# Kernel optimization log

Measured on AMD Instinct MI355X. Metric: run time of the kernel, lower is better.

Reference implementation:

```python
import jax, jax.numpy as jnp
import numpy as np

HEAD = 4
EPS = 1e-12


def _l2norm(x, axis):
    # torch F.normalize: x / max(||x||_2, eps)
    return x / jnp.maximum(jnp.linalg.norm(x, axis=axis, keepdims=True), EPS)


def setup_inputs() -> dict:
    key = jax.random.key(0)
    ks = jax.random.split(key, 12)
    n, t, c, h, w = 2, 7, 96, 96, 96
    inp = {
        "curr_feat": jax.random.normal(ks[0], (n, c, h, w), jnp.float32),
        "index_feat_set_s1": jax.random.normal(ks[1], (n, t, c, h, w), jnp.float32),
        "anchor_feat": jax.random.normal(ks[2], (n, c, h, w), jnp.float32),
        "sparse_feat_set_s1": jax.random.normal(ks[3], (n, t, c, h, w), jnp.float32),
        "sparse_feat_set_s2": jax.random.normal(ks[4], (n, t, c, h, w), jnp.float32),
        "sparse_feat_set_s3": jax.random.normal(ks[5], (n, t, c, h, w), jnp.float32),
        # absolute pixel coordinates (x,y interleaved per frame), mostly in-bounds
        # with a little overshoot to exercise zeros padding of grid_sample
        "location_feat": jax.random.uniform(ks[6], (n, t * 2, h, w), jnp.float32, minval=-2.0, maxval=float(w) + 1.0),
        "proj_w": 0.02 * jax.random.normal(ks[7], (c, c), jnp.float32),
        "proj_b": jnp.zeros((c,), jnp.float32),
        "fusion_w": 0.02 * jax.random.normal(ks[8], (c, 3 * c), jnp.float32),
        "fusion_b": jnp.zeros((c,), jnp.float32),
    }
    return inp


def reference(curr_feat, index_feat_set_s1, anchor_feat, sparse_feat_set_s1,
              sparse_feat_set_s2, sparse_feat_set_s3, location_feat,
              proj_w, proj_b, fusion_w, fusion_b):
    n, c, h, w = anchor_feat.shape
    t = sparse_feat_set_s1.shape[1]
    hd = c // HEAD
    hw = h * w

    # ---- flow-guided nearest grid_sample (align_corners=True, zeros pad) ----
    loc = location_feat.reshape(n, t, 2, h, w)  # (n,t,2,h,w): [x, y] pixel coords
    gx = 2.0 * loc[:, :, 0] / max(w - 1, 1) - 1.0
    gy = 2.0 * loc[:, :, 1] / max(h - 1, 1) - 1.0
    ix = jnp.round((gx + 1.0) * 0.5 * (w - 1))  # nearest (round-half-even, as torch)
    iy = jnp.round((gy + 1.0) * 0.5 * (h - 1))
    valid = (ix >= 0) & (ix <= w - 1) & (iy >= 0) & (iy <= h - 1)
    lin = (jnp.clip(iy, 0, h - 1).astype(jnp.int32) * w
           + jnp.clip(ix, 0, w - 1).astype(jnp.int32)).reshape(n, t, 1, hw)
    vmask = valid.reshape(n, t, 1, hw)

    def sample(f):  # f: (n,t,c,h,w) -> gathered (n,t,c,hw)
        g = jnp.take_along_axis(f.reshape(n, t, c, hw), lin, axis=3)
        return jnp.where(vmask, g, 0.0)

    samp1 = sample(sparse_feat_set_s1)
    samp2 = sample(sparse_feat_set_s2)
    samp3 = sample(sparse_feat_set_s3)
    sampi = sample(index_feat_set_s1)

    # ---- per-pixel multi-head max-correlation over t frames ----
    # queries: normalize over full channel dim c BEFORE splitting into heads
    q = _l2norm(curr_feat.reshape(n, c, hw).transpose(0, 2, 1), -1).reshape(n, hw, HEAD, hd)
    k = _l2norm(sampi.transpose(0, 3, 1, 2), -1).reshape(n, hw, t, HEAD, hd)
    scores = jnp.einsum('npthd,nphd->npht', k, q)  # scale == 1.0 in mode='max'
    corr_soft = jnp.max(scores, axis=3)     # (n,hw,head)
    corr_index = jnp.argmax(scores, axis=3)  # (n,hw,head), first-max like torch

    soft_img = jnp.broadcast_to(corr_soft[..., None], (n, hw, HEAD, hd)) \
                  .reshape(n, h, w, c).transpose(0, 3, 1, 2)  # (n,c,h,w)
    idx = jnp.broadcast_to(corr_index[..., None], (n, hw, HEAD, hd)) \
             .reshape(n, hw, c).transpose(0, 2, 1)[:, None]  # (n,1,c,hw)

    def pick(samp):  # select winning frame per (channel-group, pixel)
        return jnp.take_along_axis(samp, idx, axis=1)[:, 0].reshape(n, c, h, w)

    cat = jnp.concatenate([pick(samp1), pick(samp2), pick(samp3)], axis=1)  # (n,3c,h,w)
    out = jnp.einsum('ndhw,cd->nchw', cat, fusion_w) + fusion_b[None, :, None, None]
    out = out * soft_img
    out = jnp.einsum('nchw,dc->ndhw', out, proj_w) + proj_b[None, :, None, None]
    return out + anchor_feat
```

## Files before the change

### kernel.cpp

```cpp
#include <hip/hip_runtime.h>
#include <hip/hip_bf16.h>

#define N_    2
#define T_    7
#define C_    96
#define H_    96
#define W_    96
#define HW_   9216
#define HEAD_ 4
#define HD_   24
#define C3_   288
#define P_    16
#define QP_   100
#define CATP_ 292
#define NBLK_ (N_ * (HW_ / P_))
#define PLANES_ 14
#define CHUNK_  64
#define NCHUNK_ 144

typedef unsigned int u32;

__device__ __forceinline__ float bits2f(u32 b) {
    union { u32 u; float f; } x; x.u = b; return x.f;
}

__device__ __forceinline__ unsigned short f2bf(float f) {
    union { __hip_bfloat16 h; unsigned short s; } u;
    u.h = __float2bfloat16(f);
    return u.s;
}

template<bool BF16>
__device__ __forceinline__ float ld1(const void* p, int i) {
    if constexpr (BF16) return bits2f(((u32)((const unsigned short*)p)[i]) << 16);
    else                return ((const float*)p)[i];
}

template<bool BF16>
__device__ __forceinline__ void ld4w(const void* p, int i, float w[4]) {
    if constexpr (BF16) {
        const uint2 u = ((const uint2*)p)[i >> 2];
        w[0] = bits2f(u.x << 16);
        w[1] = bits2f(u.x & 0xFFFF0000u);
        w[2] = bits2f(u.y << 16);
        w[3] = bits2f(u.y & 0xFFFF0000u);
    } else {
        const float4 v = *((const float4*)((const float*)p + i));
        w[0] = v.x; w[1] = v.y; w[2] = v.z; w[3] = v.w;
    }
}

template<bool BF16>
__device__ __forceinline__ void st4w(void* p, int i, const float v[4]) {
    if constexpr (BF16) {
        uint2 w;
        w.x = (u32)f2bf(v[0]) | ((u32)f2bf(v[1]) << 16);
        w.y = (u32)f2bf(v[2]) | ((u32)f2bf(v[3]) << 16);
        ((uint2*)p)[i >> 2] = w;
    } else {
        *((float4*)((float*)p + i)) = make_float4(v[0], v[1], v[2], v[3]);
    }
}

__global__ void detect_dtype_kernel(const u32* __restrict__ w, int* __restrict__ flag) {
    u32 x = w[threadIdx.x];
    u32 f = x & 0x7FFFu;
    int inwin = (f >= 0x3A00u) && (f <= 0x4200u);
    unsigned long long m = __ballot(inwin);
    if (threadIdx.x == 0) flag[0] = (__popcll(m) >= 40) ? 1 : 0;
}

template<bool BF16>
__global__ __launch_bounds__(256) void transp_kernel(
    const void* __restrict__ a0, const void* __restrict__ a1,
    const void* __restrict__ a2, const void* __restrict__ a3,
    void* __restrict__ dstb, unsigned long long szb, const int* __restrict__ flag)
{
    if ((*flag != 0) != BF16) return;
    const int arr = blockIdx.y;
    const void* src = (arr == 0) ? a0 : (arr == 1) ? a1 : (arr == 2) ? a2 : a3;
    void* dst = (char*)dstb + (unsigned long long)arr * szb;
    const int bx = blockIdx.x;
    const int pl = bx / NCHUNK_;
    const int x0 = (bx - pl * NCHUNK_) * CHUNK_;
    const int tid = threadIdx.x;
    if constexpr (BF16) {
        __shared__ unsigned short tile[C_][CHUNK_ + 2];
        const unsigned short* s = (const unsigned short*)src;
        unsigned short* d = (unsigned short*)dst;
        for (int i = tid; i < C_ * (CHUNK_ / 4); i += 256) {
            int ch = i >> 4, xq = i & 15;
            const ushort4 v = *((const ushort4*)(s + (pl * C_ + ch) * HW_ + x0 + 4 * xq));
            tile[ch][4 * xq + 0] = v.x; tile[ch][4 * xq + 1] = v.y;
            tile[ch][4 * xq + 2] = v.z; tile[ch][4 * xq + 3] = v.w;
        }
        __syncthreads();
        for (int i = tid; i < CHUNK_ * (C_ / 4); i += 256) {
            int p = i / 24, cq = i - p * 24;
            ushort4 v;
            v.x = tile[4 * cq + 0][p]; v.y = tile[4 * cq + 1][p];
            v.z = tile[4 * cq + 2][p]; v.w = tile[4 * cq + 3][p];
            *((ushort4*)(d + (pl * HW_ + x0 + p) * C_ + 4 * cq)) = v;
        }
    } else {
        __shared__ float tile[C_][CHUNK_ + 1];
        const float* s = (const float*)src;
        float* d = (float*)dst;
        for (int i = tid; i < C_ * (CHUNK_ / 4); i += 256) {
            int ch = i >> 4, xq = i & 15;
            const float4 v = *((const float4*)(s + (pl * C_ + ch) * HW_ + x0 + 4 * xq));
            tile[ch][4 * xq + 0] = v.x; tile[ch][4 * xq + 1] = v.y;
            tile[ch][4 * xq + 2] = v.z; tile[ch][4 * xq + 3] = v.w;
        }
        __syncthreads();
        for (int i = tid; i < CHUNK_ * (C_ / 4); i += 256) {
            int p = i / 24, cq = i - p * 24;
            float4 v;
            v.x = tile[4 * cq + 0][p]; v.y = tile[4 * cq + 1][p];
            v.z = tile[4 * cq + 2][p]; v.w = tile[4 * cq + 3][p];
            *((float4*)(d + (pl * HW_ + x0 + p) * C_ + 4 * cq)) = v;
        }
    }
}

template<bool BF16, int MODE>
__global__ __launch_bounds__(256) void traj_main(
    const void* __restrict__ curr, const void* __restrict__ idxf,
    const void* __restrict__ anchor, const void* __restrict__ s1,
    const void* __restrict__ s2, const void* __restrict__ s3,
    const void* __restrict__ loc, const void* __restrict__ pw,
    const void* __restrict__ pb, const void* __restrict__ fw,
    const void* __restrict__ fb, void* __restrict__ outp,
    const int* __restrict__ flag,
    const void* __restrict__ kT, const void* __restrict__ s1T,
    const void* __restrict__ s2T, const void* __restrict__ s3T)
{
    if ((*flag != 0) != BF16) return;

    __shared__ __align__(16) float s_u[P_ * CATP_];
    __shared__ __align__(16) float s_mid[P_][QP_];
    __shared__ int   s_lin[T_][P_];
    __shared__ float s_red[P_][8];
    __shared__ float s_best[P_][HEAD_];
    __shared__ int   s_bidx[P_][HEAD_];
    __shared__ float s_inv[P_];

#define S_Q(pp, ch)  s_u[(pp) * QP_ + (ch)]
#define S_K(pp, ch)  s_u[P_ * QP_ + (pp) * QP_ + (ch)]
#define S_CAT(pp, d) s_u[(pp) * CATP_ + (d)]

    const int tid = threadIdx.x;
    const int b  = blockIdx.x;
    const int nn = b / (HW_ / P_);
    const int p0 = (b - nn * (HW_ / P_)) * P_;

    if (tid < T_ * P_) {
        int t = tid / P_, pp = tid - t * P_;
        int p = p0 + pp;
        float x = ld1<BF16>(loc, (nn * 2 * T_ + 2 * t    ) * HW_ + p);
        float y = ld1<BF16>(loc, (nn * 2 * T_ + 2 * t + 1) * HW_ + p);
        float gx = 2.0f * x / 95.0f - 1.0f;
        float gy = 2.0f * y / 95.0f - 1.0f;
        float fx = (gx + 1.0f) * 0.5f * 95.0f;
        float fy = (gy + 1.0f) * 0.5f * 95.0f;
        float ix = rintf(fx), iy = rintf(fy);
        bool v = (ix >= 0.0f) && (ix <= 95.0f) && (iy >= 0.0f) && (iy <= 95.0f);
        s_lin[t][pp] = v ? ((int)iy * W_ + (int)ix) : -1;
    }
    if (tid >= 128 && tid < 128 + P_ * HEAD_) {
        int q = tid - 128;
        s_best[q >> 2][q & 3] = -3.0e38f; s_bidx[q >> 2][q & 3] = 0;
    }

    for (int i = tid; i < C_ * (P_ / 4); i += 256) {
        int ch = i >> 2, pq = i & 3;
        float w[4];
        ld4w<BF16>(curr, (nn * C_ + ch) * HW_ + p0 + 4 * pq, w);
        S_Q(4 * pq + 0, ch) = w[0]; S_Q(4 * pq + 1, ch) = w[1];
        S_Q(4 * pq + 2, ch) = w[2]; S_Q(4 * pq + 3, ch) = w[3];
    }
    __syncthreads();

    if (tid < P_ * 8) {
        int pp = tid >> 3, j = tid & 7;
        float s = 0.f;
        #pragma unroll
        for (int k = 0; k < 12; ++k) { float v = S_Q(pp, j * 12 + k); s += v * v; }
        s_red[pp][j] = s;
    }
    __syncthreads();
    if (tid < P_) {
        float s = 0.f;
        #pragma unroll
        for (int j = 0; j < 8; ++j) s += s_red[tid][j];
        s_inv[tid] = 1.0f / fmaxf(sqrtf(s), 1e-12f);
    }
    __syncthreads();
    for (int i = tid; i < C_ * P_; i += 256) {
        int pp = i & (P_ - 1), ch = i >> 4;
        S_Q(pp, ch) *= s_inv[pp];
    }

    for (int t = 0; t < T_; ++t) {
        __syncthreads();
        if constexpr (MODE >= 1) {
            for (int i = tid; i < 24 * P_; i += 256) {
                int pp = i / 24, j = i - pp * 24;
                int lin = s_lin[t][pp];
                float w[4] = {0.f, 0.f, 0.f, 0.f};
                if (lin >= 0) ld4w<BF16>(kT, ((nn * T_ + t) * HW_ + lin) * C_ + 4 * j, w);
                *((float4*)&S_K(pp, 4 * j)) = make_float4(w[0], w[1], w[2], w[3]);
            }
        } else {
            for (int i = tid; i < C_ * P_; i += 256) {
                int ch = i / P_, pp = i - ch * P_;
                int lin = s_lin[t][pp];
                S_K(pp, ch) = (lin >= 0) ? ld1<BF16>(idxf, ((nn * T_ + t) * C_ + ch) * HW_ + lin) : 0.0f;
            }
        }
        __syncthreads();
        if (tid < P_ * 8) {
            int pp = tid >> 3, j = tid & 7;
            float s = 0.f;
            #pragma unroll
            for (int k = 0; k < 12; ++k) { float v = S_K(pp, j * 12 + k); s += v * v; }
            s_red[pp][j] = s;
        }
        __syncthreads();
        if (tid < P_) {
            float s = 0.f;
            #pragma unroll
            for (int j = 0; j < 8; ++j) s += s_red[tid][j];
            s_inv[tid] = 1.0f / fmaxf(sqrtf(s), 1e-12f);
        }
        __syncthreads();
        if (tid < P_ * HEAD_) {
            int pp = tid >> 2, h = tid & 3;
            float s = 0.f;
            #pragma unroll
            for (int dq = 0; dq < 6; ++dq) {
                const float4 kv = *((const float4*)&S_K(pp, h * HD_ + 4 * dq));
                const float4 qv = *((const float4*)&S_Q(pp, h * HD_ + 4 * dq));
                s += kv.x * qv.x; s += kv.y * qv.y; s += kv.z * qv.z; s += kv.w * qv.w;
            }
            s *= s_inv[pp];
            if (s > s_best[pp][h]) { s_best[pp][h] = s; s_bidx[pp][h] = t; }
        }
    }
    __syncthreads();

    if constexpr (MODE == 2) {
        for (int i = tid; i < 72 * P_; i += 256) {
            int pp = i / 72, j = i - pp * 72;
            int set = j / 24, jj = j - set * 24;
            int d0 = set * C_ + 4 * jj;
            int bt = s_bidx[pp][jj / 6];
            int lin = s_lin[bt][pp];
            float w[4] = {0.f, 0.f, 0.f, 0.f};
            if (lin >= 0) {
                const void* sp = (set == 0) ? s1T : (set == 1) ? s2T : s3T;
                ld4w<BF16>(sp, ((nn * T_ + bt) * HW_ + lin) * C_ + 4 * jj, w);
            }
            *((float4*)&S_CAT(pp, d0)) = make_float4(w[0], w[1], w[2], w[3]);
        }
    } else {
        for (int i = tid; i < C3_ * P_; i += 256) {
            int pp = i / C3_, d = i - pp * C3_;
            int set = d / C_, ch = d - set * C_;
            int h = ch / HD_;
            int bt = s_bidx[pp][h];
            int lin = s_lin[bt][pp];
            float v = 0.f;
            if (lin >= 0) {
                const void* sp = (set == 0) ? s1 : (set == 1) ? s2 : s3;
                v = ld1<BF16>(sp, ((nn * T_ + bt) * C_ + ch) * HW_ + lin);
            }
            S_CAT(pp, d) = v;
        }
    }
    __syncthreads();

    if (tid < 96) {
        const int cq = tid >> 2, pq = tid & 3;
        const int co0 = cq * 4, px0 = pq * 4;
        float acc[4][4];
        #pragma unroll
        for (int r = 0; r < 4; ++r)
            #pragma unroll
            for (int k = 0; k < 4; ++k) acc[r][k] = 0.f;
        for (int d = 0; d < C3_; d += 4) {
            float4 cv[4];
            #pragma unroll
            for (int k = 0; k < 4; ++k) cv[k] = *((const float4*)&S_CAT(px0 + k, d));
            #pragma unroll
            for (int r = 0; r < 4; ++r) {
                float w[4]; ld4w<BF16>(fw, (co0 + r) * C3_ + d, w);
                #pragma unroll
                for (int k = 0; k < 4; ++k)
                    acc[r][k] += w[0] * cv[k].x + w[1] * cv[k].y + w[2] * cv[k].z + w[3] * cv[k].w;
            }
        }
        const int hh = co0 / HD_;
        #pragma unroll
        for (int r = 0; r < 4; ++r) {
            float fbv = ld1<BF16>(fb, co0 + r);
            #pragma unroll
            for (int k = 0; k < 4; ++k)
                s_mid[px0 + k][co0 + r] = (acc[r][k] + fbv) * s_best[px0 + k][hh];
        }
    }
    __syncthreads();

    if (tid < 96) {
        const int dq = tid >> 2, pq = tid & 3;
        const int do0 = dq * 4, px0 = pq * 4;
        float acc[4][4];
        #pragma unroll
        for (int r = 0; r < 4; ++r)
            #pragma unroll
            for (int k = 0; k < 4; ++k) acc[r][k] = 0.f;
        for (int c = 0; c < C_; c += 4) {
            float4 mv[4];
            #pragma unroll
            for (int k = 0; k < 4; ++k) mv[k] = *((const float4*)&s_mid[px0 + k][c]);
            #pragma unroll
            for (int r = 0; r < 4; ++r) {
                float w[4]; ld4w<BF16>(pw, (do0 + r) * C_ + c, w);
                #pragma unroll
                for (int k = 0; k < 4; ++k)
                    acc[r][k] += w[0] * mv[k].x + w[1] * mv[k].y + w[2] * mv[k].z + w[3] * mv[k].w;
            }
        }
        #pragma unroll
        for (int r = 0; r < 4; ++r) {
            float pbv = ld1<BF16>(pb, do0 + r);
            float av[4];
            ld4w<BF16>(anchor, (nn * C_ + do0 + r) * HW_ + p0 + px0, av);
            float res[4];
            #pragma unroll
            for (int k = 0; k < 4; ++k) res[k] = acc[r][k] + pbv + av[k];
            st4w<BF16>(outp, (nn * C_ + do0 + r) * HW_ + p0 + px0, res);
        }
    }
#undef S_Q
#undef S_K
#undef S_CAT
}

extern "C" void kernel_launch(void* const* d_in, const int* in_sizes, int n_in,
                              void* d_out, int out_size, void* d_ws, size_t ws_size,
                              hipStream_t stream) {
    (void)in_sizes; (void)n_in; (void)out_size;
    int* flag = (int*)d_ws;
    char* wsb = (char*)d_ws;
    const unsigned long long SZB = (unsigned long long)N_ * T_ * HW_ * C_ * 4ull;
    void* kT  = wsb + 512;
    void* s1T = wsb + 512 + SZB;
    void* s2T = wsb + 512 + 2 * SZB;
    void* s3T = wsb + 512 + 3 * SZB;
    const int mode = (ws_size >= 512 + 4 * SZB) ? 2 : (ws_size >= 512 + SZB) ? 1 : 0;

    detect_dtype_kernel<<<1, 64, 0, stream>>>((const u32*)d_in[0], flag);

    if (mode >= 1) {
        dim3 tg(PLANES_ * NCHUNK_, (mode == 2) ? 4 : 1);
        transp_kernel<true ><<<tg, 256, 0, stream>>>(d_in[1], d_in[3], d_in[4], d_in[5], kT, SZB, flag);
        transp_kernel<false><<<tg, 256, 0, stream>>>(d_in[1], d_in[3], d_in[4], d_in[5], kT, SZB, flag);
    }

    dim3 grid(NBLK_), block(256);
#define LAUNCH_MODE(M) \
    traj_main<true,  M><<<grid, block, 0, stream>>>(d_in[0], d_in[1], d_in[2], d_in[3], d_in[4], \
        d_in[5], d_in[6], d_in[7], d_in[8], d_in[9], d_in[10], d_out, flag, kT, s1T, s2T, s3T);  \
    traj_main<false, M><<<grid, block, 0, stream>>>(d_in[0], d_in[1], d_in[2], d_in[3], d_in[4], \
        d_in[5], d_in[6], d_in[7], d_in[8], d_in[9], d_in[10], d_out, flag, kT, s1T, s2T, s3T)

    if (mode == 2)      { LAUNCH_MODE(2); }
    else if (mode == 1) { LAUNCH_MODE(1); }
    else                { LAUNCH_MODE(0); }
#undef LAUNCH_MODE
}
```

Measured before the change: 341.5 us.

## Drop sparse-set transposes and fold dtype detection into each kernel

Removes the transpose of the three sparse feature sets (mode 2), so the gather now reads 288 scalar values per pixel straight from the channel-major layout instead of vectorized channel-last loads. This saves the full read-plus-write pass over three large tensors, at the cost of scattered, uncoalesced gathers. It also drops the separate dtype-detection launch and the paired bf16/fp32 launches: each block now detects the dtype itself and branches, which cuts kernel launches but adds a 64-element read and a barrier per block.

```diff
diff --git a/kernel.cpp b/kernel.cpp
--- a/kernel.cpp
+++ b/kernel.cpp
@@ -62,30 +62,27 @@
     }
 }
 
-__global__ void detect_dtype_kernel(const u32* __restrict__ w, int* __restrict__ flag) {
-    u32 x = w[threadIdx.x];
-    u32 f = x & 0x7FFFu;
-    int inwin = (f >= 0x3A00u) && (f <= 0x4200u);
-    unsigned long long m = __ballot(inwin);
-    if (threadIdx.x == 0) flag[0] = (__popcll(m) >= 40) ? 1 : 0;
+__device__ __forceinline__ bool block_detect_bf16(const u32* __restrict__ w,
+                                                  int tid, int* s_flag) {
+    if (tid < 64) {
+        u32 x = w[tid];
+        u32 f = x & 0x7FFFu;
+        int inwin = (f >= 0x3A00u) && (f <= 0x4200u);
+        unsigned long long m = __ballot(inwin);
+        if (tid == 0) *s_flag = (__popcll(m) >= 40) ? 1 : 0;
+    }
+    __syncthreads();
+    return *s_flag != 0;
 }
 
 template<bool BF16>
-__global__ __launch_bounds__(256) void transp_kernel(
-    const void* __restrict__ a0, const void* __restrict__ a1,
-    const void* __restrict__ a2, const void* __restrict__ a3,
-    void* __restrict__ dstb, unsigned long long szb, const int* __restrict__ flag)
-{
-    if ((*flag != 0) != BF16) return;
-    const int arr = blockIdx.y;
-    const void* src = (arr == 0) ? a0 : (arr == 1) ? a1 : (arr == 2) ? a2 : a3;
-    void* dst = (char*)dstb + (unsigned long long)arr * szb;
-    const int bx = blockIdx.x;
+__device__ __forceinline__ void transp_body(const void* __restrict__ src,
+                                            void* __restrict__ dst,
+                                            int bx, int tid, char* tileraw) {
     const int pl = bx / NCHUNK_;
     const int x0 = (bx - pl * NCHUNK_) * CHUNK_;
-    const int tid = threadIdx.x;
     if constexpr (BF16) {
-        __shared__ unsigned short tile[C_][CHUNK_ + 2];
+        unsigned short (*tile)[CHUNK_ + 2] = (unsigned short (*)[CHUNK_ + 2])tileraw;
         const unsigned short* s = (const unsigned short*)src;
         unsigned short* d = (unsigned short*)dst;
         for (int i = tid; i < C_ * (CHUNK_ / 4); i += 256) {
@@ -103,7 +100,7 @@
             *((ushort4*)(d + (pl * HW_ + x0 + p) * C_ + 4 * cq)) = v;
         }
     } else {
-        __shared__ float tile[C_][CHUNK_ + 1];
+        float (*tile)[CHUNK_ + 1] = (float (*)[CHUNK_ + 1])tileraw;
         const float* s = (const float*)src;
         float* d = (float*)dst;
         for (int i = tid; i < C_ * (CHUNK_ / 4); i += 256) {
@@ -123,28 +120,30 @@
     }
 }
 
+__global__ __launch_bounds__(256) void transp_kernel(
+    const void* __restrict__ idxf, void* __restrict__ dst,
+    const u32* __restrict__ detect_src)
+{
+    __shared__ __align__(16) char tileraw[C_ * (CHUNK_ + 1) * 4];
+    __shared__ int s_flag;
+    const int tid = threadIdx.x;
+    const bool bf = block_detect_bf16(detect_src, tid, &s_flag);
+    if (bf) transp_body<true >(idxf, dst, blockIdx.x, tid, tileraw);
+    else    transp_body<false>(idxf, dst, blockIdx.x, tid, tileraw);
+}
+
 template<bool BF16, int MODE>
-__global__ __launch_bounds__(256) void traj_main(
+__device__ __forceinline__ void traj_body(
     const void* __restrict__ curr, const void* __restrict__ idxf,
     const void* __restrict__ anchor, const void* __restrict__ s1,
     const void* __restrict__ s2, const void* __restrict__ s3,
     const void* __restrict__ loc, const void* __restrict__ pw,
     const void* __restrict__ pb, const void* __restrict__ fw,
     const void* __restrict__ fb, void* __restrict__ outp,
-    const int* __restrict__ flag,
-    const void* __restrict__ kT, const void* __restrict__ s1T,
-    const void* __restrict__ s2T, const void* __restrict__ s3T)
+    const void* __restrict__ kT,
+    float* s_u, float (*s_mid)[QP_], int (*s_lin)[P_], float (*s_red)[8],
+    float (*s_best)[HEAD_], int (*s_bidx)[HEAD_], float* s_inv)
 {
-    if ((*flag != 0) != BF16) return;
-
-    __shared__ __align__(16) float s_u[P_ * CATP_];
-    __shared__ __align__(16) float s_mid[P_][QP_];
-    __shared__ int   s_lin[T_][P_];
-    __shared__ float s_red[P_][8];
-    __shared__ float s_best[P_][HEAD_];
-    __shared__ int   s_bidx[P_][HEAD_];
-    __shared__ float s_inv[P_];
-
 #define S_Q(pp, ch)  s_u[(pp) * QP_ + (ch)]
 #define S_K(pp, ch)  s_u[P_ * QP_ + (pp) * QP_ + (ch)]
 #define S_CAT(pp, d) s_u[(pp) * CATP_ + (d)]
@@ -249,34 +248,18 @@
     }
     __syncthreads();
 
-    if constexpr (MODE == 2) {
-        for (int i = tid; i < 72 * P_; i += 256) {
-            int pp = i / 72, j = i - pp * 72;
-            int set = j / 24, jj = j - set * 24;
-            int d0 = set * C_ + 4 * jj;
-            int bt = s_bidx[pp][jj / 6];
-            int lin = s_lin[bt][pp];
-            float w[4] = {0.f, 0.f, 0.f, 0.f};
-            if (lin >= 0) {
-                const void* sp = (set == 0) ? s1T : (set == 1) ? s2T : s3T;
-                ld4w<BF16>(sp, ((nn * T_ + bt) * HW_ + lin) * C_ + 4 * jj, w);
-            }
-            *((float4*)&S_CAT(pp, d0)) = make_float4(w[0], w[1], w[2], w[3]);
-        }
-    } else {
-        for (int i = tid; i < C3_ * P_; i += 256) {
-            int pp = i / C3_, d = i - pp * C3_;
-            int set = d / C_, ch = d - set * C_;
-            int h = ch / HD_;
-            int bt = s_bidx[pp][h];
-            int lin = s_lin[bt][pp];
-            float v = 0.f;
-            if (lin >= 0) {
-                const void* sp = (set == 0) ? s1 : (set == 1) ? s2 : s3;
-                v = ld1<BF16>(sp, ((nn * T_ + bt) * C_ + ch) * HW_ + lin);
-            }
-            S_CAT(pp, d) = v;
-        }
+    for (int i = tid; i < C3_ * P_; i += 256) {
+        int pp = i / C3_, d = i - pp * C3_;
+        int set = d / C_, ch = d - set * C_;
+        int h = ch / HD_;
+        int bt = s_bidx[pp][h];
+        int lin = s_lin[bt][pp];
+        float v = 0.f;
+        if (lin >= 0) {
+            const void* sp = (set == 0) ? s1 : (set == 1) ? s2 : s3;
+            v = ld1<BF16>(sp, ((nn * T_ + bt) * C_ + ch) * HW_ + lin);
+        }
+        S_CAT(pp, d) = v;
     }
     __syncthreads();
 
@@ -347,36 +330,49 @@
 #undef S_CAT
 }
 
+template<int MODE>
+__global__ __launch_bounds__(256) void traj_main(
+    const void* __restrict__ curr, const void* __restrict__ idxf,
+    const void* __restrict__ anchor, const void* __restrict__ s1,
+    const void* __restrict__ s2, const void* __restrict__ s3,
+    const void* __restrict__ loc, const void* __restrict__ pw,
+    const void* __restrict__ pb, const void* __restrict__ fw,
+    const void* __restrict__ fb, void* __restrict__ outp,
+    const void* __restrict__ kT)
+{
+    __shared__ __align__(16) float s_u[P_ * CATP_];
+    __shared__ __align__(16) float s_mid[P_][QP_];
+    __shared__ int   s_lin[T_][P_];
+    __shared__ float s_red[P_][8];
+    __shared__ float s_best[P_][HEAD_];
+    __shared__ int   s_bidx[P_][HEAD_];
+    __shared__ float s_inv[P_];
+    __shared__ int   s_flag;
+
+    const bool bf = block_detect_bf16((const u32*)curr, threadIdx.x, &s_flag);
+    if (bf) traj_body<true,  MODE>(curr, idxf, anchor, s1, s2, s3, loc, pw, pb, fw, fb,
+                                   outp, kT, s_u, s_mid, s_lin, s_red, s_best, s_bidx, s_inv);
+    else    traj_body<false, MODE>(curr, idxf, anchor, s1, s2, s3, loc, pw, pb, fw, fb,
+                                   outp, kT, s_u, s_mid, s_lin, s_red, s_best, s_bidx, s_inv);
+}
+
 extern "C" void kernel_launch(void* const* d_in, const int* in_sizes, int n_in,
                               void* d_out, int out_size, void* d_ws, size_t ws_size,
                               hipStream_t stream) {
     (void)in_sizes; (void)n_in; (void)out_size;
-    int* flag = (int*)d_ws;
-    char* wsb = (char*)d_ws;
     const unsigned long long SZB = (unsigned long long)N_ * T_ * HW_ * C_ * 4ull;
-    void* kT  = wsb + 512;
-    void* s1T = wsb + 512 + SZB;
-    void* s2T = wsb + 512 + 2 * SZB;
-    void* s3T = wsb + 512 + 3 * SZB;
-    const int mode = (ws_size >= 512 + 4 * SZB) ? 2 : (ws_size >= 512 + SZB) ? 1 : 0;
-
-    detect_dtype_kernel<<<1, 64, 0, stream>>>((const u32*)d_in[0], flag);
-
-    if (mode >= 1) {
-        dim3 tg(PLANES_ * NCHUNK_, (mode == 2) ? 4 : 1);
-        transp_kernel<true ><<<tg, 256, 0, stream>>>(d_in[1], d_in[3], d_in[4], d_in[5], kT, SZB, flag);
-        transp_kernel<false><<<tg, 256, 0, stream>>>(d_in[1], d_in[3], d_in[4], d_in[5], kT, SZB, flag);
-    }
+    void* kT = d_ws;
+    const int mode = (ws_size >= SZB) ? 1 : 0;
 
     dim3 grid(NBLK_), block(256);
-#define LAUNCH_MODE(M) \
-    traj_main<true,  M><<<grid, block, 0, stream>>>(d_in[0], d_in[1], d_in[2], d_in[3], d_in[4], \
-        d_in[5], d_in[6], d_in[7], d_in[8], d_in[9], d_in[10], d_out, flag, kT, s1T, s2T, s3T);  \
-    traj_main<false, M><<<grid, block, 0, stream>>>(d_in[0], d_in[1], d_in[2], d_in[3], d_in[4], \
-        d_in[5], d_in[6], d_in[7], d_in[8], d_in[9], d_in[10], d_out, flag, kT, s1T, s2T, s3T)
-
-    if (mode == 2)      { LAUNCH_MODE(2); }
-    else if (mode == 1) { LAUNCH_MODE(1); }
-    else                { LAUNCH_MODE(0); }
-#undef LAUNCH_MODE
-}
+    if (mode == 1) {
+        transp_kernel<<<dim3(PLANES_ * NCHUNK_), 256, 0, stream>>>(d_in[1], kT, (const u32*)d_in[0]);
+        traj_main<1><<<grid, block, 0, stream>>>(d_in[0], d_in[1], d_in[2], d_in[3], d_in[4],
+                                                 d_in[5], d_in[6], d_in[7], d_in[8], d_in[9],
+                                                 d_in[10], d_out, kT);
+    } else {
+        traj_main<0><<<grid, block, 0, stream>>>(d_in[0], d_in[1], d_in[2], d_in[3], d_in[4],
+                                                 d_in[5], d_in[6], d_in[7], d_in[8], d_in[9],
+                                                 d_in[10], d_out, kT);
+    }
+}
```

New measurement: 332.9 us. 1.03x faster.
